# Optimization experiments

Hardware: AMD Instinct MI355X
Metric: run time of the kernel (lower is better)

The kernel has to match this reference:

```python
import jax, jax.numpy as jnp
import numpy as np

CLUSTERS = 128
ITERATIONS = 10
TOPK = 32
NEG = -1e7


def setup_inputs() -> dict:
    key = jax.random.key(0)
    k1, k2, k3, k4 = jax.random.split(key, 4)
    N, L, H, E = 2, 2048, 8, 64
    BITS = 32
    return {
        "queries": jax.random.normal(k1, (N, L, H, E), dtype=jnp.float32),
        "keys": jax.random.normal(k2, (N, L, H, E), dtype=jnp.float32),
        "values": jax.random.normal(k3, (N, L, H, E), dtype=jnp.float32),
        "planes": jax.random.normal(k4, (BITS, E + 1), dtype=jnp.float32),
    }


def _cluster(bits, C, iterations):
    # bits: [N,H,L,B] in {0,1}. Lloyd k-means under Hamming distance.
    N, H, L, B = bits.shape
    init_idx = (np.arange(C) * L) // C
    cent = bits[:, :, init_idx, :]  # [N,H,C,B]
    for _ in range(iterations):
        # hamming(b,c) = b.(1-c) + (1-b).c
        d = (jnp.einsum('nhlb,nhcb->nhlc', bits, 1.0 - cent)
             + jnp.einsum('nhlb,nhcb->nhlc', 1.0 - bits, cent))
        assign = jnp.argmin(d, axis=-1)                      # [N,H,L]
        oh = jax.nn.one_hot(assign, C, dtype=jnp.float32)    # [N,H,L,C]
        cnt = oh.sum(axis=2)                                 # [N,H,C]
        sums = jnp.einsum('nhlc,nhlb->nhcb', oh, bits)
        new = (sums / jnp.maximum(cnt, 1.0)[..., None] >= 0.5).astype(jnp.float32)
        cent = jnp.where((cnt > 0.0)[..., None], new, cent)
    d = (jnp.einsum('nhlb,nhcb->nhlc', bits, 1.0 - cent)
         + jnp.einsum('nhlb,nhcb->nhlc', 1.0 - bits, cent))
    assign = jnp.argmin(d, axis=-1)
    oh = jax.nn.one_hot(assign, C, dtype=jnp.float32)
    cnt = oh.sum(axis=2)
    return assign, oh, cnt


def _forward(queries, keys, values, planes):
    # to [N,H,L,E]
    Q = jnp.transpose(queries, (0, 2, 1, 3))
    K = jnp.transpose(keys, (0, 2, 1, 3))
    V = jnp.transpose(values, (0, 2, 1, 3))
    N, H, L, E = Q.shape
    S = K.shape[2]
    temp = 1.0 / np.sqrt(E)

    # --- hash queries with random hyperplanes (bias column: hash_bias=True) ---
    x = jnp.concatenate([Q, jnp.ones(Q.shape[:-1] + (1,), Q.dtype)], axis=-1)
    bits = (jnp.einsum('nhle,be->nhlb', x, planes) > 0).astype(jnp.float32)

    # --- cluster queries (Lloyd on hamming distance over hash bits) ---
    assign, oh, cnt = _cluster(bits, CLUSTERS, ITERATIONS)

    # --- per-cluster centroid queries (mean over members) ---
    Qg = jnp.einsum('nhlc,nhle->nhce', oh, Q) / jnp.maximum(cnt, 1.0)[..., None]

    # --- top-k keys per cluster ---
    QKc = jnp.einsum('nhce,nhse->nhcs', Qg, K)   # [N,H,C,S]
    k = min(TOPK, S)
    _, tki = jax.lax.top_k(QKc, k)               # [N,H,C,k]

    # broadcast each cluster's top-k indices to its member queries
    idx_q = jnp.take_along_axis(
        tki, jnp.broadcast_to(assign[:, :, :, None], (N, H, L, k)), axis=2)  # [N,H,L,k]

    gather = jax.vmap(jax.vmap(lambda a, i: a[i]))
    K_sel = gather(K, idx_q)                     # [N,H,L,k,E]
    V_sel = gather(V, idx_q)                     # [N,H,L,k,E]

    qk = jnp.einsum('nhle,nhlke->nhlk', Q, K_sel)
    future = idx_q > jnp.arange(L)[None, None, :, None]   # causal: key pos > query pos
    qk = jnp.where(future, NEG, qk)
    A = jax.nn.softmax(temp * qk, axis=-1)
    A = A * (1.0 - future.astype(A.dtype))
    out = jnp.einsum('nhlk,nhlkd->nhld', A, V_sel)
    return jnp.transpose(out, (0, 2, 1, 3))      # [N,L,H,D]


def reference(queries, keys, values, planes):
    return _forward(queries, keys, values, planes)
```

## Files before the change

kernel.cpp:

```cpp
#include <hip/hip_runtime.h>
#include <math.h>

#define NB 2
#define HB 8
#define LB 2048
#define EB 64
#define BITSN 32
#define CLN 128
#define ITERS 10
#define TOPKN 32
#define NEGV -10000000.0f

typedef unsigned long long u64;
typedef unsigned int u32;

#define PART_NH16 (33 * 64)
#define PART_ITER16 (NB * HB * PART_NH16)
#define PART_TOTAL16 (ITERS * PART_ITER16)
#define BITS_BLOCKS 4096
#define ZBLOCKS ((PART_TOTAL16 + 255) / 256)

__global__ __launch_bounds__(256) void bits_zero_kernel(const float* __restrict__ q,
                                                        const float* __restrict__ planes,
                                                        u32* __restrict__ bits,
                                                        u32* __restrict__ zbuf) {
    int tid = threadIdx.x;
    int bid = blockIdx.x;
    if (bid >= BITS_BLOCKS) {
        int i = (bid - BITS_BLOCKS) * 256 + tid;
        if (i < PART_TOTAL16) zbuf[i] = 0u;
        return;
    }
    int wave = tid >> 6;
    int lane = tid & 63;
    int b = lane & 31;
    int which = lane >> 5;
    int qi = bid * 8 + wave * 2 + which;
    int l = qi & (LB - 1);
    int nh = qi / LB;
    int h = nh & (HB - 1);
    int n = nh / HB;
    const float* qrow = q + (((long long)n * LB + l) * HB + h) * EB;
    const float* prow = planes + b * (EB + 1);
    double acc = (double)prow[EB];
    #pragma unroll 8
    for (int e = 0; e < EB; ++e) acc += (double)qrow[e] * (double)prow[e];
    unsigned long long m = __ballot(acc > 0.0);
    if (b == 0) {
        bits[qi] = (u32)(which ? (m >> 32) : (m & 0xffffffffULL));
    }
}

__global__ __launch_bounds__(256) void kmeans_iter_kernel(const u32* __restrict__ bits,
                                                          const u32* __restrict__ part_prev,
                                                          u32* __restrict__ part_cur,
                                                          const u32* __restrict__ cent_prev_g,
                                                          u32* __restrict__ cent_cur_g,
                                                          int it) {
    __shared__ u32 cent[CLN];
    __shared__ int hist[33 * 128];
    int tid = threadIdx.x;
    int bid = blockIdx.x;
    int nh = bid >> 3;
    int tile = bid & 7;
    int lane = tid & 63;

    for (int i = tid; i < 33 * 128; i += 256) hist[i] = 0;
    if (tid < CLN) {
        u32 cv;
        if (it == 0) {
            cv = bits[nh * LB + tid * (LB / CLN)];
        } else {
            const u32* pp = part_prev + nh * PART_NH16;
            int sh = (tid & 1) * 16;
            int cnt = (int)((pp[32 * 64 + (tid >> 1)] >> sh) & 0xffffu);
            u32 nb = 0u;
            #pragma unroll
            for (int j = 0; j < BITSN; ++j) {
                int s = (int)((pp[j * 64 + (tid >> 1)] >> sh) & 0xffffu);
                if (2 * s >= cnt) nb |= (1u << j);
            }
            cv = (cnt > 0) ? nb : cent_prev_g[nh * CLN + tid];
        }
        cent[tid] = cv;
        if (tile == 0) cent_cur_g[nh * CLN + tid] = cv;
    }
    __syncthreads();

    int l = tile * 256 + tid;
    u32 bv = bits[nh * LB + l];

    u32 clo = cent[lane], chi = cent[lane + 64];
    u32 best = 0x7fffffffu;
    #pragma unroll 16
    for (int c = 0; c < 64; ++c) {
        u32 cc = (u32)__builtin_amdgcn_readlane((int)clo, c);
        u32 key = ((u32)__popc(bv ^ cc) << 7) | (u32)c;
        best = (key < best) ? key : best;
    }
    #pragma unroll 16
    for (int c = 0; c < 64; ++c) {
        u32 cc = (u32)__builtin_amdgcn_readlane((int)chi, c);
        u32 key = ((u32)__popc(bv ^ cc) << 7) | (u32)(64 + c);
        best = (key < best) ? key : best;
    }
    int bc = (int)(best & 127u);

    atomicAdd(&hist[32 * 128 + bc], 1);
    u32 bb = bv;
    while (bb) { int j = __ffs(bb) - 1; atomicAdd(&hist[j * 128 + bc], 1); bb &= bb - 1; }
    __syncthreads();

    u32* pc = part_cur + nh * PART_NH16;
    for (int i = tid; i < PART_NH16; i += 256) {
        int j = i >> 6, p = i & 63;
        u32 v = (u32)hist[j * 128 + 2 * p] | ((u32)hist[j * 128 + 2 * p + 1] << 16);
        if (v) atomicAdd(&pc[i], v);
    }
}

__global__ __launch_bounds__(1024) void list_final_kernel(const u32* __restrict__ bits,
                                                          const u32* __restrict__ part_prev,
                                                          const u32* __restrict__ cent_prev_g,
                                                          int* __restrict__ csort_g,
                                                          int* __restrict__ cnt_g,
                                                          int* __restrict__ ofs_g,
                                                          int* __restrict__ list_g) {
    __shared__ u32 cent[CLN];
    __shared__ int cnt[CLN];
    __shared__ int cntw[2][16][CLN];
    __shared__ int ofs[CLN];
    int nh = blockIdx.x;
    int tid = threadIdx.x;
    int w = tid >> 6, lane = tid & 63;

    if (tid < CLN) {
        const u32* pp = part_prev + nh * PART_NH16;
        int sh = (tid & 1) * 16;
        int cn = (int)((pp[32 * 64 + (tid >> 1)] >> sh) & 0xffffu);
        u32 nb = 0u;
        #pragma unroll
        for (int j = 0; j < BITSN; ++j) {
            int s = (int)((pp[j * 64 + (tid >> 1)] >> sh) & 0xffffu);
            if (2 * s >= cn) nb |= (1u << j);
        }
        cent[tid] = (cn > 0) ? nb : cent_prev_g[nh * CLN + tid];
        cnt[tid] = 0;
    }
    for (int i = tid; i < 2 * 16 * CLN; i += 1024) (&cntw[0][0][0])[i] = 0;
    __syncthreads();

    int l0 = tid, l1 = tid + 1024;
    u32 bv0 = bits[nh * LB + l0];
    u32 bv1 = bits[nh * LB + l1];
    u32 clo = cent[lane], chi = cent[lane + 64];
    u32 best0 = 0x7fffffffu, best1 = 0x7fffffffu;
    #pragma unroll 16
    for (int c = 0; c < 64; ++c) {
        u32 cc = (u32)__builtin_amdgcn_readlane((int)clo, c);
        u32 k0 = ((u32)__popc(bv0 ^ cc) << 7) | (u32)c;
        u32 k1 = ((u32)__popc(bv1 ^ cc) << 7) | (u32)c;
        best0 = (k0 < best0) ? k0 : best0;
        best1 = (k1 < best1) ? k1 : best1;
    }
    #pragma unroll 16
    for (int c = 0; c < 64; ++c) {
        u32 cc = (u32)__builtin_amdgcn_readlane((int)chi, c);
        u32 k0 = ((u32)__popc(bv0 ^ cc) << 7) | (u32)(64 + c);
        u32 k1 = ((u32)__popc(bv1 ^ cc) << 7) | (u32)(64 + c);
        best0 = (k0 < best0) ? k0 : best0;
        best1 = (k1 < best1) ? k1 : best1;
    }
    int bc0 = (int)(best0 & 127u);
    int bc1 = (int)(best1 & 127u);
    u64 ltmask = (lane == 0) ? 0ULL : (~0ULL >> (64 - lane));

    int rank0 = 0, rank1 = 0;
    for (int c = 0; c < CLN; ++c) {
        u64 m0 = __ballot(bc0 == c);
        u64 m1 = __ballot(bc1 == c);
        if ((m0 | m1) == 0ULL) continue;
        if (bc0 == c) rank0 = (int)__popcll(m0 & ltmask);
        if (bc1 == c) rank1 = (int)__popcll(m1 & ltmask);
        if (lane == 0) {
            int p0 = (int)__popcll(m0), p1 = (int)__popcll(m1);
            if (p0) cntw[0][w][c] = p0;
            if (p1) cntw[1][w][c] = p1;
            atomicAdd(&cnt[c], p0 + p1);
        }
    }
    __syncthreads();
    if (tid == 0) {
        int run = 0;
        for (int c = 0; c < CLN; ++c) { ofs[c] = run; run += cnt[c]; }
    }
    __syncthreads();
    if (tid < CLN) {
        int c = tid;
        int run = ofs[c];
        #pragma unroll
        for (int g = 0; g < 2; ++g)
            for (int ww = 0; ww < 16; ++ww) {
                int t = cntw[g][ww][c];
                cntw[g][ww][c] = run;
                run += t;
            }
        cnt_g[nh * CLN + c] = cnt[c];
        ofs_g[nh * CLN + c] = ofs[c];
    }
    __syncthreads();
    {
        int p0 = cntw[0][w][bc0] + rank0;
        int p1 = cntw[1][w][bc1] + rank1;
        list_g[nh * LB + p0] = l0;
        list_g[nh * LB + p1] = l1;
        csort_g[nh * LB + p0] = bc0;
        csort_g[nh * LB + p1] = bc1;
    }
}

__global__ __launch_bounds__(256) void qg_kernel(const float* __restrict__ q,
                                                 const int* __restrict__ cnt_g,
                                                 const int* __restrict__ ofs_g,
                                                 const int* __restrict__ list_g,
                                                 float* __restrict__ qgf) {
    __shared__ double ps[4][EB];
    int bid = blockIdx.x;
    int nh = bid >> 7;
    int h = nh & (HB - 1);
    int n = nh / HB;
    int tid = threadIdx.x;
    int w = tid >> 6, lane = tid & 63;
    int cn = cnt_g[bid];
    int o = ofs_g[bid];
    const int* lp = list_g + nh * LB + o;
    double acc = 0.0;
    for (int i = w; i < cn; i += 4) {
        int l = lp[i];
        acc += (double)q[(((long long)n * LB + l) * HB + h) * EB + lane];
    }
    ps[w][lane] = acc;
    __syncthreads();
    if (tid < EB) {
        double s = ((ps[0][tid] + ps[1][tid]) + ps[2][tid]) + ps[3][tid];
        double dcn = (double)(cn > 0 ? cn : 1);
        qgf[(long long)bid * EB + tid] = (float)(s / dcn);
    }
}

__global__ __launch_bounds__(256) void scores_topsel_kernel(const float* __restrict__ kk,
                                                            const float* __restrict__ qgf,
                                                            int* __restrict__ tki_g) {
    __shared__ float qs[8 * EB];
    __shared__ u32 skey[8][LB];
    int bid = blockIdx.x;
    int nh = bid >> 4;
    int g = bid & 15;
    int cbase = g * 8;
    int h = nh & (HB - 1);
    int n = nh / HB;
    int tid = threadIdx.x;
    int w = tid >> 6, lane = tid & 63;

    if (tid < 128)
        ((float4*)qs)[tid] = ((const float4*)(qgf + (long long)(nh * CLN + cbase) * EB))[tid];
    __syncthreads();

    for (int step = 0; step < 8; ++step) {
        int l = step * 256 + tid;
        const float4* kr4 = (const float4*)(kk + (((long long)n * LB + l) * HB + h) * EB);
        float rr[EB];
        #pragma unroll
        for (int i = 0; i < 16; ++i) {
            float4 t4 = kr4[i];
            rr[4 * i] = t4.x; rr[4 * i + 1] = t4.y; rr[4 * i + 2] = t4.z; rr[4 * i + 3] = t4.w;
        }
        #pragma unroll
        for (int c = 0; c < 8; ++c) {
            const float4* qp = (const float4*)(qs + c * EB);
            float a0 = 0.f, a1 = 0.f, a2 = 0.f, a3 = 0.f;
            #pragma unroll
            for (int i = 0; i < 4; ++i) {
                float4 q0 = qp[i], q1 = qp[4 + i], q2 = qp[8 + i], q3 = qp[12 + i];
                int e0 = 4 * i, e1 = 16 + 4 * i, e2 = 32 + 4 * i, e3 = 48 + 4 * i;
                a0 = fmaf(q0.x, rr[e0], a0); a0 = fmaf(q0.y, rr[e0 + 1], a0);
                a0 = fmaf(q0.z, rr[e0 + 2], a0); a0 = fmaf(q0.w, rr[e0 + 3], a0);
                a1 = fmaf(q1.x, rr[e1], a1); a1 = fmaf(q1.y, rr[e1 + 1], a1);
                a1 = fmaf(q1.z, rr[e1 + 2], a1); a1 = fmaf(q1.w, rr[e1 + 3], a1);
                a2 = fmaf(q2.x, rr[e2], a2); a2 = fmaf(q2.y, rr[e2 + 1], a2);
                a2 = fmaf(q2.z, rr[e2 + 2], a2); a2 = fmaf(q2.w, rr[e2 + 3], a2);
                a3 = fmaf(q3.x, rr[e3], a3); a3 = fmaf(q3.y, rr[e3 + 1], a3);
                a3 = fmaf(q3.z, rr[e3 + 2], a3); a3 = fmaf(q3.w, rr[e3 + 3], a3);
            }
            float acc = (a0 + a1) + (a2 + a3);
            u32 u = __float_as_uint(acc);
            u = ((int)u < 0) ? ~u : (u | 0x80000000u);
            skey[c][l] = u;
        }
    }
    __syncthreads();

    for (int rep = 0; rep < 2; ++rep) {
        int c = w + rep * 4;
        const uint4* kp4 = (const uint4*)&skey[c][0];
        u64 k[32];
        #pragma unroll
        for (int t = 0; t < 8; ++t) {
            uint4 kv = kp4[lane + 64 * t];
            int l0 = (lane + 64 * t) * 4;
            k[4 * t]     = ((u64)kv.x << 32) | (u32)(2047 - l0);
            k[4 * t + 1] = ((u64)kv.y << 32) | (u32)(2047 - (l0 + 1));
            k[4 * t + 2] = ((u64)kv.z << 32) | (u32)(2047 - (l0 + 2));
            k[4 * t + 3] = ((u64)kv.w << 32) | (u32)(2047 - (l0 + 3));
        }
        u64 m0 = k[0], m1 = k[8], m2 = k[16], m3 = k[24];
        #pragma unroll
        for (int t = 1; t < 8; ++t) {
            if (k[t] > m0) m0 = k[t];
            if (k[8 + t] > m1) m1 = k[8 + t];
            if (k[16 + t] > m2) m2 = k[16 + t];
            if (k[24 + t] > m3) m3 = k[24 + t];
        }
        if (m1 > m0) m0 = m1;
        if (m3 > m2) m2 = m3;
        u64 cur = (m2 > m0) ? m2 : m0;
        for (int r = 0; r < TOPKN; ++r) {
            u64 wk = cur;
            #pragma unroll
            for (int off = 1; off < 64; off <<= 1) {
                u64 o = __shfl_xor(wk, off);
                if (o > wk) wk = o;
            }
            if (lane == 0)
                tki_g[(nh * CLN + cbase + c) * TOPKN + r] = 2047 - (int)(wk & 2047u);
            if (wk == cur) {
                u64 nm = 0ULL;
                #pragma unroll
                for (int t = 0; t < 32; ++t) {
                    u64 kt = k[t];
                    u64 cand = (kt < wk) ? kt : 0ULL;
                    if (cand > nm) nm = cand;
                }
                cur = nm;
            }
        }
    }
}

__device__ __forceinline__ void attn_one(const float* __restrict__ q,
                                         const float* __restrict__ kk,
                                         const float* __restrict__ vv,
                                         int n, int h, int l,
                                         const int* __restrict__ krow,
                                         int lane, float* __restrict__ out) {
    int j = lane & 31, p = lane >> 5;
    int kidx = krow[j];
    const float* vbase = vv + ((long long)n * LB * HB + h) * EB;
    float vreg[TOPKN];
    #pragma unroll
    for (int jj = 0; jj < TOPKN; ++jj) {
        int kj = __shfl(kidx, jj);
        vreg[jj] = vbase[(long long)kj * (HB * EB) + lane];
    }
    const float4* q4 = (const float4*)(q + (((long long)n * LB + l) * HB + h) * EB) + p * 8;
    const float4* k4 = (const float4*)(kk + (((long long)n * LB + kidx) * HB + h) * EB) + p * 8;
    float part = 0.f;
    #pragma unroll
    for (int i = 0; i < 8; ++i) {
        float4 a = q4[i], b = k4[i];
        part += a.x * b.x + a.y * b.y + a.z * b.z + a.w * b.w;
    }
    float qlo = __shfl(part, j);
    float qhi = __shfl(part, j + 32);
    float qk = qlo + qhi;
    bool future = kidx > l;
    float logit = 0.125f * (future ? NEGV : qk);
    float m = logit;
    #pragma unroll
    for (int off = 16; off; off >>= 1) m = fmaxf(m, __shfl_xor(m, off));
    float ex = expf(logit - m);
    float ssum = ex;
    #pragma unroll
    for (int off = 16; off; off >>= 1) ssum += __shfl_xor(ssum, off);
    float a = future ? 0.f : ex / ssum;
    float oacc = 0.f;
    #pragma unroll
    for (int jj = 0; jj < TOPKN; ++jj) {
        float aj = __shfl(a, jj);
        oacc = fmaf(aj, vreg[jj], oacc);
    }
    out[(((long long)n * LB + l) * HB + h) * EB + lane] = oacc;
}

__device__ __forceinline__ void attn_pair_body(const float* __restrict__ q,
                                               const float* __restrict__ kk,
                                               const float* __restrict__ vv,
                                               int n, int h, int l0, int l1,
                                               const int* __restrict__ krow,
                                               int lane, float* __restrict__ out) {
    int j = lane & 31, p = lane >> 5;
    int kidx = krow[j];
    const float* vbase = vv + ((long long)n * LB * HB + h) * EB;
    float vreg[TOPKN];
    #pragma unroll
    for (int jj = 0; jj < TOPKN; ++jj) {
        int kj = __shfl(kidx, jj);
        vreg[jj] = vbase[(long long)kj * (HB * EB) + lane];
    }
    const float4* q40 = (const float4*)(q + (((long long)n * LB + l0) * HB + h) * EB) + p * 8;
    const float4* q41 = (const float4*)(q + (((long long)n * LB + l1) * HB + h) * EB) + p * 8;
    const float4* k4  = (const float4*)(kk + (((long long)n * LB + kidx) * HB + h) * EB) + p * 8;
    float part0 = 0.f, part1 = 0.f;
    #pragma unroll
    for (int i = 0; i < 8; ++i) {
        float4 b = k4[i];
        float4 a0 = q40[i], a1 = q41[i];
        part0 += a0.x * b.x + a0.y * b.y + a0.z * b.z + a0.w * b.w;
        part1 += a1.x * b.x + a1.y * b.y + a1.z * b.z + a1.w * b.w;
    }
    float qk0 = __shfl(part0, j) + __shfl(part0, j + 32);
    float qk1 = __shfl(part1, j) + __shfl(part1, j + 32);
    bool fut0 = kidx > l0, fut1 = kidx > l1;
    float lg0 = 0.125f * (fut0 ? NEGV : qk0);
    float lg1 = 0.125f * (fut1 ? NEGV : qk1);
    float m0 = lg0, m1 = lg1;
    #pragma unroll
    for (int off = 16; off; off >>= 1) {
        m0 = fmaxf(m0, __shfl_xor(m0, off));
        m1 = fmaxf(m1, __shfl_xor(m1, off));
    }
    float e0 = expf(lg0 - m0), e1 = expf(lg1 - m1);
    float s0 = e0, s1 = e1;
    #pragma unroll
    for (int off = 16; off; off >>= 1) {
        s0 += __shfl_xor(s0, off);
        s1 += __shfl_xor(s1, off);
    }
    float a0 = fut0 ? 0.f : e0 / s0;
    float a1 = fut1 ? 0.f : e1 / s1;
    float o0 = 0.f, o1 = 0.f;
    #pragma unroll
    for (int jj = 0; jj < TOPKN; ++jj) {
        float aj0 = __shfl(a0, jj);
        float aj1 = __shfl(a1, jj);
        o0 = fmaf(aj0, vreg[jj], o0);
        o1 = fmaf(aj1, vreg[jj], o1);
    }
    out[(((long long)n * LB + l0) * HB + h) * EB + lane] = o0;
    out[(((long long)n * LB + l1) * HB + h) * EB + lane] = o1;
}

__global__ __launch_bounds__(256) void attn_quad_kernel(const float* __restrict__ q,
                                                        const float* __restrict__ kk,
                                                        const float* __restrict__ vv,
                                                        const int* __restrict__ list_g,
                                                        const int* __restrict__ csort_g,
                                                        const int* __restrict__ tki_g,
                                                        float* __restrict__ out) {
    int tid = threadIdx.x;
    int wave = tid >> 6, lane = tid & 63;
    int idx = blockIdx.x * 4 + wave;
    int nh = idx >> 9;
    int qd = idx & 511;
    int pos = 4 * qd;
    int l0 = list_g[nh * LB + pos];
    int l1 = list_g[nh * LB + pos + 1];
    int l2 = list_g[nh * LB + pos + 2];
    int l3 = list_g[nh * LB + pos + 3];
    int c0 = csort_g[nh * LB + pos];
    int c1 = csort_g[nh * LB + pos + 1];
    int c2 = csort_g[nh * LB + pos + 2];
    int c3 = csort_g[nh * LB + pos + 3];
    int h = nh & (HB - 1);
    int n = nh / HB;

    if ((c0 != c1) | (c1 != c2) | (c2 != c3)) {
        if (c0 == c1) {
            attn_pair_body(q, kk, vv, n, h, l0, l1, tki_g + (nh * CLN + c0) * TOPKN, lane, out);
        } else {
            attn_one(q, kk, vv, n, h, l0, tki_g + (nh * CLN + c0) * TOPKN, lane, out);
            attn_one(q, kk, vv, n, h, l1, tki_g + (nh * CLN + c1) * TOPKN, lane, out);
        }
        if (c2 == c3) {
            attn_pair_body(q, kk, vv, n, h, l2, l3, tki_g + (nh * CLN + c2) * TOPKN, lane, out);
        } else {
            attn_one(q, kk, vv, n, h, l2, tki_g + (nh * CLN + c2) * TOPKN, lane, out);
            attn_one(q, kk, vv, n, h, l3, tki_g + (nh * CLN + c3) * TOPKN, lane, out);
        }
        return;
    }

    const int* krow = tki_g + (nh * CLN + c0) * TOPKN;
    int j = lane & 31, p = lane >> 5;
    int kidx = krow[j];
    const float* vbase = vv + ((long long)n * LB * HB + h) * EB;
    float vreg[TOPKN];
    #pragma unroll
    for (int jj = 0; jj < TOPKN; ++jj) {
        int kj = __shfl(kidx, jj);
        vreg[jj] = vbase[(long long)kj * (HB * EB) + lane];
    }

    const float4* q40 = (const float4*)(q + (((long long)n * LB + l0) * HB + h) * EB) + p * 8;
    const float4* q41 = (const float4*)(q + (((long long)n * LB + l1) * HB + h) * EB) + p * 8;
    const float4* q42 = (const float4*)(q + (((long long)n * LB + l2) * HB + h) * EB) + p * 8;
    const float4* q43 = (const float4*)(q + (((long long)n * LB + l3) * HB + h) * EB) + p * 8;
    const float4* k4  = (const float4*)(kk + (((long long)n * LB + kidx) * HB + h) * EB) + p * 8;
    float p0 = 0.f, p1 = 0.f, p2 = 0.f, p3 = 0.f;
    #pragma unroll
    for (int i = 0; i < 8; ++i) {
        float4 b = k4[i];
        float4 a0 = q40[i], a1 = q41[i], a2 = q42[i], a3 = q43[i];
        p0 += a0.x * b.x + a0.y * b.y + a0.z * b.z + a0.w * b.w;
        p1 += a1.x * b.x + a1.y * b.y + a1.z * b.z + a1.w * b.w;
        p2 += a2.x * b.x + a2.y * b.y + a2.z * b.z + a2.w * b.w;
        p3 += a3.x * b.x + a3.y * b.y + a3.z * b.z + a3.w * b.w;
    }
    float qk0 = __shfl(p0, j) + __shfl(p0, j + 32);
    float qk1 = __shfl(p1, j) + __shfl(p1, j + 32);
    float qk2 = __shfl(p2, j) + __shfl(p2, j + 32);
    float qk3 = __shfl(p3, j) + __shfl(p3, j + 32);

    bool f0 = kidx > l0, f1 = kidx > l1, f2 = kidx > l2, f3 = kidx > l3;
    float g0 = 0.125f * (f0 ? NEGV : qk0);
    float g1 = 0.125f * (f1 ? NEGV : qk1);
    float g2 = 0.125f * (f2 ? NEGV : qk2);
    float g3 = 0.125f * (f3 ? NEGV : qk3);
    float m0 = g0, m1 = g1, m2 = g2, m3 = g3;
    #pragma unroll
    for (int off = 16; off; off >>= 1) {
        m0 = fmaxf(m0, __shfl_xor(m0, off));
        m1 = fmaxf(m1, __shfl_xor(m1, off));
        m2 = fmaxf(m2, __shfl_xor(m2, off));
        m3 = fmaxf(m3, __shfl_xor(m3, off));
    }
    float e0 = expf(g0 - m0), e1 = expf(g1 - m1);
    float e2 = expf(g2 - m2), e3 = expf(g3 - m3);
    float s0 = e0, s1 = e1, s2 = e2, s3 = e3;
    #pragma unroll
    for (int off = 16; off; off >>= 1) {
        s0 += __shfl_xor(s0, off);
        s1 += __shfl_xor(s1, off);
        s2 += __shfl_xor(s2, off);
        s3 += __shfl_xor(s3, off);
    }
    float a0 = f0 ? 0.f : e0 / s0;
    float a1 = f1 ? 0.f : e1 / s1;
    float a2 = f2 ? 0.f : e2 / s2;
    float a3 = f3 ? 0.f : e3 / s3;

    float o0 = 0.f, o1 = 0.f, o2 = 0.f, o3 = 0.f;
    #pragma unroll
    for (int jj = 0; jj < TOPKN; ++jj) {
        float v = vreg[jj];
        o0 = fmaf(__shfl(a0, jj), v, o0);
        o1 = fmaf(__shfl(a1, jj), v, o1);
        o2 = fmaf(__shfl(a2, jj), v, o2);
        o3 = fmaf(__shfl(a3, jj), v, o3);
    }
    out[(((long long)n * LB + l0) * HB + h) * EB + lane] = o0;
    out[(((long long)n * LB + l1) * HB + h) * EB + lane] = o1;
    out[(((long long)n * LB + l2) * HB + h) * EB + lane] = o2;
    out[(((long long)n * LB + l3) * HB + h) * EB + lane] = o3;
}

extern "C" void kernel_launch(void* const* d_in, const int* in_sizes, int n_in,
                              void* d_out, int out_size, void* d_ws, size_t ws_size,
                              hipStream_t stream) {
    const float* q = (const float*)d_in[0];
    const float* k = (const float*)d_in[1];
    const float* v = (const float*)d_in[2];
    const float* planes = (const float*)d_in[3];
    float* out = (float*)d_out;

    const int NQ = NB * HB * LB;
    char* ws = (char*)d_ws;
    u32* bits     = (u32*)(ws);
    int* csort_g  = (int*)(ws + 0x20000);
    int* cnt_g    = (int*)(ws + 0x40000);
    int* ofs_g    = (int*)(ws + 0x42000);
    int* list_g   = (int*)(ws + 0x44000);
    float* qgf    = (float*)(ws + 0x64000);
    int* tki_g    = (int*)(ws + 0xE4000);
    u32* part_all = (u32*)(ws + 0x124000);
    u32* cents0   = (u32*)(ws + 0x124000 + 0x180000);
    u32* cents1   = (u32*)(ws + 0x124000 + 0x182000);

    bits_zero_kernel<<<BITS_BLOCKS + ZBLOCKS, 256, 0, stream>>>(q, planes, bits, part_all);

    for (int it = 0; it < ITERS; ++it) {
        const u32* pp = part_all + (it == 0 ? 0 : (it - 1)) * PART_ITER16;
        u32* pc       = part_all + it * PART_ITER16;
        const u32* cprev = (it & 1) ? cents0 : cents1;
        u32* ccur        = (it & 1) ? cents1 : cents0;
        kmeans_iter_kernel<<<NB * HB * 8, 256, 0, stream>>>(bits, pp, pc, cprev, ccur, it);
    }
    list_final_kernel<<<NB * HB, 1024, 0, stream>>>(
        bits, part_all + 9 * PART_ITER16, cents1, csort_g, cnt_g, ofs_g, list_g);
    qg_kernel<<<NB * HB * CLN, 256, 0, stream>>>(q, cnt_g, ofs_g, list_g, qgf);
    scores_topsel_kernel<<<NB * HB * 16, 256, 0, stream>>>(k, qgf, tki_g);
    attn_quad_kernel<<<NQ / 16, 256, 0, stream>>>(q, k, v, list_g, csort_g, tki_g, out);
}
```

Measured before the change: 276.3 us.

## Split fused cluster scoring and top-k selection into two kernels

Replaces the fused scores+top-k kernel (256 blocks each holding 8 clusters' score rows in 64KB of shared memory) with a scores kernel that tiles over key positions and writes sortable keys to global memory, followed by a 64-thread-per-cluster top-k kernel launched over all 4096 clusters. This raises parallelism and occupancy by removing the large shared-memory footprint and the serial per-wave top-k loops. In exchange it adds a global round-trip of the 2048x2048 key matrix per head pair (about 32MB total) and an extra launch. The keys buffer reuses the workspace region of the k-means partials, which are no longer needed at that point.

```diff
diff --git a/kernel.cpp b/kernel.cpp
--- a/kernel.cpp
+++ b/kernel.cpp
@@ -248,101 +248,104 @@
     }
 }
 
-__global__ __launch_bounds__(256) void scores_topsel_kernel(const float* __restrict__ kk,
-                                                            const float* __restrict__ qgf,
-                                                            int* __restrict__ tki_g) {
-    __shared__ float qs[8 * EB];
-    __shared__ u32 skey[8][LB];
+__global__ __launch_bounds__(256) void scores_kernel(const float* __restrict__ kk,
+                                                     const float* __restrict__ qgf,
+                                                     u32* __restrict__ keys) {
+    __shared__ float qs[CLN * EB];
     int bid = blockIdx.x;
-    int nh = bid >> 4;
-    int g = bid & 15;
-    int cbase = g * 8;
+    int nh = bid >> 5;
+    int tile = bid & 31;
     int h = nh & (HB - 1);
     int n = nh / HB;
     int tid = threadIdx.x;
-    int w = tid >> 6, lane = tid & 63;
-
-    if (tid < 128)
-        ((float4*)qs)[tid] = ((const float4*)(qgf + (long long)(nh * CLN + cbase) * EB))[tid];
-    __syncthreads();
-
-    for (int step = 0; step < 8; ++step) {
-        int l = step * 256 + tid;
-        const float4* kr4 = (const float4*)(kk + (((long long)n * LB + l) * HB + h) * EB);
-        float rr[EB];
+    int w = tid >> 6;
+    int lane = tid & 63;
+    int l = tile * 64 + lane;
+    int cbase = w * 32;
+
+    {
+        const float4* src = (const float4*)(qgf + (long long)nh * CLN * EB);
+        float4* dst = (float4*)qs;
         #pragma unroll
-        for (int i = 0; i < 16; ++i) {
-            float4 t4 = kr4[i];
-            rr[4 * i] = t4.x; rr[4 * i + 1] = t4.y; rr[4 * i + 2] = t4.z; rr[4 * i + 3] = t4.w;
-        }
+        for (int i = 0; i < 8; ++i) dst[tid + 256 * i] = src[tid + 256 * i];
+    }
+
+    const float4* kr4 = (const float4*)(kk + (((long long)n * LB + l) * HB + h) * EB);
+    float rr[EB];
+    #pragma unroll
+    for (int i = 0; i < 16; ++i) {
+        float4 t4 = kr4[i];
+        rr[4 * i] = t4.x; rr[4 * i + 1] = t4.y; rr[4 * i + 2] = t4.z; rr[4 * i + 3] = t4.w;
+    }
+    __syncthreads();
+
+    for (int c = 0; c < 32; ++c) {
+        const float4* qp = (const float4*)(qs + (cbase + c) * EB);
+        float a0 = 0.f, a1 = 0.f, a2 = 0.f, a3 = 0.f;
         #pragma unroll
-        for (int c = 0; c < 8; ++c) {
-            const float4* qp = (const float4*)(qs + c * EB);
-            float a0 = 0.f, a1 = 0.f, a2 = 0.f, a3 = 0.f;
+        for (int i = 0; i < 4; ++i) {
+            float4 q0 = qp[i], q1 = qp[4 + i], q2 = qp[8 + i], q3 = qp[12 + i];
+            int e0 = 4 * i, e1 = 16 + 4 * i, e2 = 32 + 4 * i, e3 = 48 + 4 * i;
+            a0 = fmaf(q0.x, rr[e0], a0); a0 = fmaf(q0.y, rr[e0 + 1], a0);
+            a0 = fmaf(q0.z, rr[e0 + 2], a0); a0 = fmaf(q0.w, rr[e0 + 3], a0);
+            a1 = fmaf(q1.x, rr[e1], a1); a1 = fmaf(q1.y, rr[e1 + 1], a1);
+            a1 = fmaf(q1.z, rr[e1 + 2], a1); a1 = fmaf(q1.w, rr[e1 + 3], a1);
+            a2 = fmaf(q2.x, rr[e2], a2); a2 = fmaf(q2.y, rr[e2 + 1], a2);
+            a2 = fmaf(q2.z, rr[e2 + 2], a2); a2 = fmaf(q2.w, rr[e2 + 3], a2);
+            a3 = fmaf(q3.x, rr[e3], a3); a3 = fmaf(q3.y, rr[e3 + 1], a3);
+            a3 = fmaf(q3.z, rr[e3 + 2], a3); a3 = fmaf(q3.w, rr[e3 + 3], a3);
+        }
+        float acc = (a0 + a1) + (a2 + a3);
+        u32 u = __float_as_uint(acc);
+        u = ((int)u < 0) ? ~u : (u | 0x80000000u);
+        keys[((long long)(nh * CLN + cbase + c)) * LB + l] = u;
+    }
+}
+
+__global__ __launch_bounds__(64) void topsel_kernel(const u32* __restrict__ keys,
+                                                    int* __restrict__ tki_g) {
+    int bid = blockIdx.x;
+    int lane = threadIdx.x;
+    const uint4* kp4 = (const uint4*)(keys + (long long)bid * LB);
+    u64 k[32];
+    #pragma unroll
+    for (int t = 0; t < 8; ++t) {
+        uint4 kv = kp4[lane + 64 * t];
+        int l0 = (lane + 64 * t) * 4;
+        k[4 * t]     = ((u64)kv.x << 32) | (u32)(2047 - l0);
+        k[4 * t + 1] = ((u64)kv.y << 32) | (u32)(2047 - (l0 + 1));
+        k[4 * t + 2] = ((u64)kv.z << 32) | (u32)(2047 - (l0 + 2));
+        k[4 * t + 3] = ((u64)kv.w << 32) | (u32)(2047 - (l0 + 3));
+    }
+    u64 m0 = k[0], m1 = k[8], m2 = k[16], m3 = k[24];
+    #pragma unroll
+    for (int t = 1; t < 8; ++t) {
+        if (k[t] > m0) m0 = k[t];
+        if (k[8 + t] > m1) m1 = k[8 + t];
+        if (k[16 + t] > m2) m2 = k[16 + t];
+        if (k[24 + t] > m3) m3 = k[24 + t];
+    }
+    if (m1 > m0) m0 = m1;
+    if (m3 > m2) m2 = m3;
+    u64 cur = (m2 > m0) ? m2 : m0;
+
+    for (int r = 0; r < TOPKN; ++r) {
+        u64 wk = cur;
+        #pragma unroll
+        for (int off = 1; off < 64; off <<= 1) {
+            u64 o = __shfl_xor(wk, off);
+            if (o > wk) wk = o;
+        }
+        if (lane == 0) tki_g[bid * TOPKN + r] = 2047 - (int)(wk & 2047u);
+        if (wk == cur) {
+            u64 nm = 0ULL;
             #pragma unroll
-            for (int i = 0; i < 4; ++i) {
-                float4 q0 = qp[i], q1 = qp[4 + i], q2 = qp[8 + i], q3 = qp[12 + i];
-                int e0 = 4 * i, e1 = 16 + 4 * i, e2 = 32 + 4 * i, e3 = 48 + 4 * i;
-                a0 = fmaf(q0.x, rr[e0], a0); a0 = fmaf(q0.y, rr[e0 + 1], a0);
-                a0 = fmaf(q0.z, rr[e0 + 2], a0); a0 = fmaf(q0.w, rr[e0 + 3], a0);
-                a1 = fmaf(q1.x, rr[e1], a1); a1 = fmaf(q1.y, rr[e1 + 1], a1);
-                a1 = fmaf(q1.z, rr[e1 + 2], a1); a1 = fmaf(q1.w, rr[e1 + 3], a1);
-                a2 = fmaf(q2.x, rr[e2], a2); a2 = fmaf(q2.y, rr[e2 + 1], a2);
-                a2 = fmaf(q2.z, rr[e2 + 2], a2); a2 = fmaf(q2.w, rr[e2 + 3], a2);
-                a3 = fmaf(q3.x, rr[e3], a3); a3 = fmaf(q3.y, rr[e3 + 1], a3);
-                a3 = fmaf(q3.z, rr[e3 + 2], a3); a3 = fmaf(q3.w, rr[e3 + 3], a3);
+            for (int t = 0; t < 32; ++t) {
+                u64 kt = k[t];
+                u64 cand = (kt < wk) ? kt : 0ULL;
+                if (cand > nm) nm = cand;
             }
-            float acc = (a0 + a1) + (a2 + a3);
-            u32 u = __float_as_uint(acc);
-            u = ((int)u < 0) ? ~u : (u | 0x80000000u);
-            skey[c][l] = u;
-        }
-    }
-    __syncthreads();
-
-    for (int rep = 0; rep < 2; ++rep) {
-        int c = w + rep * 4;
-        const uint4* kp4 = (const uint4*)&skey[c][0];
-        u64 k[32];
-        #pragma unroll
-        for (int t = 0; t < 8; ++t) {
-            uint4 kv = kp4[lane + 64 * t];
-            int l0 = (lane + 64 * t) * 4;
-            k[4 * t]     = ((u64)kv.x << 32) | (u32)(2047 - l0);
-            k[4 * t + 1] = ((u64)kv.y << 32) | (u32)(2047 - (l0 + 1));
-            k[4 * t + 2] = ((u64)kv.z << 32) | (u32)(2047 - (l0 + 2));
-            k[4 * t + 3] = ((u64)kv.w << 32) | (u32)(2047 - (l0 + 3));
-        }
-        u64 m0 = k[0], m1 = k[8], m2 = k[16], m3 = k[24];
-        #pragma unroll
-        for (int t = 1; t < 8; ++t) {
-            if (k[t] > m0) m0 = k[t];
-            if (k[8 + t] > m1) m1 = k[8 + t];
-            if (k[16 + t] > m2) m2 = k[16 + t];
-            if (k[24 + t] > m3) m3 = k[24 + t];
-        }
-        if (m1 > m0) m0 = m1;
-        if (m3 > m2) m2 = m3;
-        u64 cur = (m2 > m0) ? m2 : m0;
-        for (int r = 0; r < TOPKN; ++r) {
-            u64 wk = cur;
-            #pragma unroll
-            for (int off = 1; off < 64; off <<= 1) {
-                u64 o = __shfl_xor(wk, off);
-                if (o > wk) wk = o;
-            }
-            if (lane == 0)
-                tki_g[(nh * CLN + cbase + c) * TOPKN + r] = 2047 - (int)(wk & 2047u);
-            if (wk == cur) {
-                u64 nm = 0ULL;
-                #pragma unroll
-                for (int t = 0; t < 32; ++t) {
-                    u64 kt = k[t];
-                    u64 cand = (kt < wk) ? kt : 0ULL;
-                    if (cand > nm) nm = cand;
-                }
-                cur = nm;
-            }
+            cur = nm;
         }
     }
 }
@@ -582,6 +585,7 @@
     int* list_g   = (int*)(ws + 0x44000);
     float* qgf    = (float*)(ws + 0x64000);
     int* tki_g    = (int*)(ws + 0xE4000);
+    u32* keys     = (u32*)(ws + 0x124000);
     u32* part_all = (u32*)(ws + 0x124000);
     u32* cents0   = (u32*)(ws + 0x124000 + 0x180000);
     u32* cents1   = (u32*)(ws + 0x124000 + 0x182000);
@@ -598,6 +602,7 @@
     list_final_kernel<<<NB * HB, 1024, 0, stream>>>(
         bits, part_all + 9 * PART_ITER16, cents1, csort_g, cnt_g, ofs_g, list_g);
     qg_kernel<<<NB * HB * CLN, 256, 0, stream>>>(q, cnt_g, ofs_g, list_g, qgf);
-    scores_topsel_kernel<<<NB * HB * 16, 256, 0, stream>>>(k, qgf, tki_g);
+    scores_kernel<<<NB * HB * 32, 256, 0, stream>>>(k, qgf, keys);
+    topsel_kernel<<<NB * HB * CLN, 64, 0, stream>>>(keys, tki_g);
     attn_quad_kernel<<<NQ / 16, 256, 0, stream>>>(q, k, v, list_g, csort_g, tki_g, out);
 }
```

New measurement: 244.1 us. -11.6%, faster.
